# Kernel optimization log

Measured on AMD Instinct MI355X. Metric: run time of the kernel, lower is better.

The kernel has to match this reference:

```python
import jax, jax.numpy as jnp
import numpy as np
import math

DIM = 1024
N_HEADS = 16
HEAD_DIM = DIM // N_HEADS
MAX_LEN = 4096
THETA = 10000.0
LN_EPS = 1e-5


def _rope_tables(dim, max_len, theta=THETA):
    # matches precompute_rope: freqs over even indices, angles = outer(t, freqs)
    inv = 1.0 / theta ** (np.arange(0, dim, 2, dtype=np.float32) / dim)
    t = np.arange(max_len, dtype=np.float32)
    ang = np.outer(t, inv)  # [max_len, dim//2]
    return jnp.asarray(np.cos(ang)), jnp.asarray(np.sin(ang))


def setup_inputs() -> dict:
    key = jax.random.key(0)
    ks = jax.random.split(key, 5)
    B, T, D = 2, 2048, DIM
    s = 1.0 / math.sqrt(D)
    x = jax.random.normal(ks[0], (B, T, D), dtype=jnp.float32)
    wq = jax.random.normal(ks[1], (D, D), dtype=jnp.float32) * s
    wk = jax.random.normal(ks[2], (D, D), dtype=jnp.float32) * s
    wv = jax.random.normal(ks[3], (D, D), dtype=jnp.float32) * s
    wo = jax.random.normal(ks[4], (D, D), dtype=jnp.float32) * s
    ln_g = jnp.ones((D,), dtype=jnp.float32)
    ln_b = jnp.zeros((D,), dtype=jnp.float32)
    cos, sin = _rope_tables(HEAD_DIM, MAX_LEN)
    return {"x": x, "wq": wq, "wk": wk, "wv": wv, "wo": wo,
            "ln_g": ln_g, "ln_b": ln_b, "cos": cos, "sin": sin}


def _rotate(x, cos, sin):
    # x: [B, T, H, hd]; complex multiply on interleaved (even, odd) pairs
    B, T, H, hd = x.shape
    xr = x.reshape(B, T, H, hd // 2, 2)
    x0, x1 = xr[..., 0], xr[..., 1]
    c = cos[None, :T, None, :]
    s = sin[None, :T, None, :]
    o0 = x0 * c - x1 * s
    o1 = x0 * s + x1 * c
    return jnp.stack([o0, o1], axis=-1).reshape(B, T, H, hd)


def reference(x, wq, wk, wv, wo, ln_g, ln_b, cos, sin):
    B, T, D = x.shape
    H, hd = N_HEADS, HEAD_DIM
    # LayerNorm
    mu = jnp.mean(x, axis=-1, keepdims=True)
    var = jnp.var(x, axis=-1, keepdims=True)
    h = (x - mu) * jax.lax.rsqrt(var + LN_EPS) * ln_g + ln_b
    # QKV projections (torch Linear: h @ W.T)
    q = jnp.einsum('btd,ed->bte', h, wq).reshape(B, T, H, hd)
    k = jnp.einsum('btd,ed->bte', h, wk).reshape(B, T, H, hd)
    v = jnp.einsum('btd,ed->bte', h, wv).reshape(B, T, H, hd)
    q = _rotate(q, cos, sin)
    k = _rotate(k, cos, sin)
    # full (non-causal) attention, scores [B, H, T, T]
    scores = jnp.einsum('bqhd,bkhd->bhqk', q, k) / math.sqrt(hd)
    attn = jax.nn.softmax(scores, axis=-1)
    out = jnp.einsum('bhqk,bkhd->bqhd', attn, v).reshape(B, T, D)
    return jnp.einsum('btd,ed->bte', out, wo)
```

## Files before the change

kernel.cpp:

```cpp
#include <hip/hip_runtime.h>
#include <hip/hip_bf16.h>

typedef __attribute__((ext_vector_type(4))) float          fx4;
typedef __attribute__((ext_vector_type(8))) __bf16         bfx8;
typedef __attribute__((ext_vector_type(8))) unsigned short usx8;
typedef __attribute__((ext_vector_type(4))) unsigned short usx4;

#define TLEN 2048
#define ROWS 4096
#define D    1024

__device__ __forceinline__ float bf2f(unsigned short u) {
    union { unsigned int i; float f; } v; v.i = ((unsigned int)u) << 16; return v.f;
}
__device__ __forceinline__ unsigned short f2bf(float f) {
    union { float f; unsigned int i; } v; v.f = f;
    unsigned int r = v.i + 0x7fffu + ((v.i >> 16) & 1u);
    return (unsigned short)(r >> 16);
}
__device__ __forceinline__ unsigned int cvtpk_bf16(float lo, float hi) {
    unsigned int r;
    asm("v_cvt_pk_bf16_f32 %0, %1, %2" : "=v"(r) : "v"(lo), "v"(hi));
    return r;
}
__device__ __forceinline__ void gload_lds16(const unsigned short* g, unsigned short* l) {
    __builtin_amdgcn_global_load_lds((const __attribute__((address_space(1))) void*)g,
                                     (__attribute__((address_space(3))) void*)l, 16, 0, 0);
}

__device__ __forceinline__ usx4 cvt4(fx4 a) {
    usx4 o;
    #pragma unroll
    for (int j = 0; j < 4; j++) o[j] = f2bf(a[j]);
    return o;
}
__global__ __launch_bounds__(256) void prep_kernel(const float* __restrict__ x,
                                                   const float* __restrict__ g,
                                                   const float* __restrict__ bta,
                                                   const float* __restrict__ wq, const float* __restrict__ wk,
                                                   const float* __restrict__ wv, const float* __restrict__ wo,
                                                   unsigned short* __restrict__ hout,
                                                   unsigned short* __restrict__ wqkv,
                                                   unsigned short* __restrict__ wob,
                                                   float* __restrict__ ropeTab) {
    const int tid = threadIdx.x;
    if (blockIdx.x >= 5120) {
        const int idx = (blockIdx.x - 5120) * 256 + tid;
        const int pi_ = idx >> 11, t = idx & 2047;
        float inv = __builtin_amdgcn_exp2f(-0.415241011861f * (float)pi_);
        float ang = (float)t * inv;
        ropeTab[idx * 2]     = cosf(ang);
        ropeTab[idx * 2 + 1] = sinf(ang);
        return;
    }
    if (blockIdx.x >= 4096) {
        const int i = (blockIdx.x - 4096) * 256 + tid;
        ((usx4*)wqkv)[i]          = cvt4(((const fx4*)wq)[i]);
        ((usx4*)wqkv)[262144 + i] = cvt4(((const fx4*)wk)[i]);
        ((usx4*)wqkv)[524288 + i] = cvt4(((const fx4*)wv)[i]);
        ((usx4*)wob)[i]           = cvt4(((const fx4*)wo)[i]);
        return;
    }
    const int row = blockIdx.x;
    fx4 v = ((const fx4*)(x + (size_t)row * D))[tid];
    float s  = v[0] + v[1] + v[2] + v[3];
    float s2 = v[0]*v[0] + v[1]*v[1] + v[2]*v[2] + v[3]*v[3];
    #pragma unroll
    for (int mk = 32; mk >= 1; mk >>= 1) { s += __shfl_xor(s, mk); s2 += __shfl_xor(s2, mk); }
    __shared__ float red[8];
    const int wave = tid >> 6, lane = tid & 63;
    if (lane == 0) { red[wave] = s; red[4 + wave] = s2; }
    __syncthreads();
    s  = red[0] + red[1] + red[2] + red[3];
    s2 = red[4] + red[5] + red[6] + red[7];
    float mu   = s * (1.0f / D);
    float var  = s2 * (1.0f / D) - mu * mu;
    float rstd = rsqrtf(var + 1e-5f);
    fx4 gv = ((const fx4*)g)[tid];
    fx4 bv = ((const fx4*)bta)[tid];
    usx4 o;
    #pragma unroll
    for (int j = 0; j < 4; j++) o[j] = f2bf((v[j] - mu) * rstd * gv[j] + bv[j]);
    ((usx4*)hout)[(size_t)row * 256 + tid] = o;
}

__global__ __launch_bounds__(512) void qkvt_gemm(const unsigned short* __restrict__ hbuf,
                                                 const unsigned short* __restrict__ wqkv,
                                                 unsigned short* __restrict__ qkout,
                                                 unsigned short* __restrict__ vtout,
                                                 const float* __restrict__ ropeTab) {
    constexpr int K = 1024;
    __shared__ __align__(16) unsigned short As[2][256 * 64];
    __shared__ __align__(16) unsigned short Bs[2][256 * 64];
    const int tid = threadIdx.x, lane = tid & 63, wave = tid >> 6;
    const int fr = lane & 15, fq = lane >> 4;
    const int wr = wave >> 2, wc = wave & 3;

    const int id = (blockIdx.x & 7) * 24 + (blockIdx.x >> 3);
    const bool isqk = id < 128;
    int bm, bn;
    const unsigned short *Ab, *Bb;
    if (isqk) {
        bm = id & 15; bn = id >> 4;
        Ab = hbuf + (size_t)(bm * 256) * K;
        Bb = wqkv + (size_t)(bn * 256) * K;
    } else {
        int j = id - 128; bm = j & 3; bn = j >> 2;
        Ab = wqkv + (size_t)(2048 * 1024) + (size_t)(bm * 256) * K;
        Bb = hbuf + (size_t)(bn * 256) * K;
    }

    const int srow   = wave * 8 + (lane >> 3);
    const int sc_dst = (lane & 7) * 8;
    const int sc_src = ((lane & 7) ^ (lane >> 3)) * 8;

    #define STAGE_Q(BUF, KT)                                                          \
        {                                                                             \
            _Pragma("unroll")                                                         \
            for (int i = 0; i < 4; i++) {                                             \
                const int r = srow + 64 * i;                                          \
                gload_lds16(Ab + (size_t)r * K + (KT) + sc_src, &As[BUF][r * 64 + sc_dst]); \
                gload_lds16(Bb + (size_t)r * K + (KT) + sc_src, &Bs[BUF][r * 64 + sc_dst]); \
            }                                                                         \
        }

    fx4 acc[8][4];
    #pragma unroll
    for (int m = 0; m < 8; m++)
        #pragma unroll
        for (int n = 0; n < 4; n++) acc[m][n] = (fx4)0.0f;

    STAGE_Q(0, 0)

    #pragma unroll 2
    for (int kt = 0; kt < K; kt += 64) {
        const int b = (kt >> 6) & 1;
        __syncthreads();
        if (kt + 64 < K) STAGE_Q(b ^ 1, kt + 64)
        #pragma unroll
        for (int s = 0; s < 2; s++) {
            bfx8 aF[8], bF[4];
            #pragma unroll
            for (int m = 0; m < 8; m++)
                aF[m] = *(const bfx8*)&As[b][(wr * 128 + m * 16 + fr) * 64 + (((s * 4 + fq) ^ (fr & 7)) * 8)];
            #pragma unroll
            for (int n = 0; n < 4; n++)
                bF[n] = *(const bfx8*)&Bs[b][(wc * 64 + n * 16 + fr) * 64 + (((s * 4 + fq) ^ (fr & 7)) * 8)];
            #pragma unroll
            for (int m = 0; m < 8; m++)
                #pragma unroll
                for (int n = 0; n < 4; n++)
                    acc[m][n] = __builtin_amdgcn_mfma_f32_16x16x32_bf16(aF[m], bF[n], acc[m][n], 0, 0, 0);
        }
    }
    #undef STAGE_Q

    const int row0 = bm * 256 + wr * 128 + fq * 4;
    const int col0 = bn * 256 + wc * 64 + fr;
    if (isqk) {
        const float QS = 0.125f * 1.44269504088896f;
        const bool isq = bn < 4;
        const float sgn = (fr & 1) ? 1.0f : -1.0f;
        #pragma unroll
        for (int m = 0; m < 8; m++) {
            const int rbase = row0 + m * 16;
            const int tb = rbase & (TLEN - 1);
            #pragma unroll
            for (int n = 0; n < 4; n++) {
                const float* tp = ropeTab + ((((n * 8 + (fr >> 1)) << 11) | tb) << 1);
                fx4 csA = *(const fx4*)tp;
                fx4 csB = *(const fx4*)(tp + 4);
                #pragma unroll
                for (int j = 0; j < 4; j++) {
                    float c  = (j < 2) ? csA[2 * j]     : csB[2 * (j - 2)];
                    float s_ = (j < 2) ? csA[2 * j + 1] : csB[2 * (j - 2) + 1];
                    float self = acc[m][n][j];
                    float other = __shfl_xor(self, 1);
                    float o = self * c + other * (sgn * s_);
                    if (isq) o *= QS;
                    qkout[(size_t)(rbase + j) * 2048 + col0 + n * 16] = f2bf(o);
                }
            }
        }
    } else {
        const int bb = bn >> 3;
        #pragma unroll
        for (int m = 0; m < 8; m++)
            #pragma unroll
            for (int n = 0; n < 4; n++) {
                const int t = (col0 + n * 16) & (TLEN - 1);
                const int tp = (t & ~63) | ((n >> 1) * 32 + ((fr >> 2)) * 8 + ((n & 1)) * 4 + (fr & 3));
                #pragma unroll
                for (int j = 0; j < 4; j++) {
                    const int d = row0 + m * 16 + j;
                    vtout[(((size_t)(bb * 16 + (d >> 6)) * 64) + (d & 63)) * TLEN + tp] = f2bf(acc[m][n][j]);
                }
            }
    }
}

__global__ __launch_bounds__(256) void gemm_out64(const unsigned short* __restrict__ A,
                                                  const unsigned short* __restrict__ B,
                                                  float* __restrict__ C) {
    constexpr int K = 1024;
    __shared__ __align__(16) unsigned short As[128 * 64];
    __shared__ __align__(16) unsigned short Bs[64 * 64];
    const int tid = threadIdx.x, lane = tid & 63, wave = tid >> 6;
    const int fr = lane & 15, fq = lane >> 4;
    const int bm = blockIdx.x, bn = blockIdx.y;
    const int wr = wave >> 1, wc = wave & 1;

    const int srow   = wave * 8 + (lane >> 3);
    const int sc_dst = (lane & 7) * 8;
    const int sc_src = ((lane & 7) ^ (lane >> 3)) * 8;
    const unsigned short* Ab = A + (size_t)(bm * 128) * K;
    const unsigned short* Bb = B + (size_t)(bn * 64) * K;

    fx4 acc[4][2];
    #pragma unroll
    for (int m = 0; m < 4; m++)
        #pragma unroll
        for (int n = 0; n < 2; n++) acc[m][n] = (fx4)0.0f;

    for (int kt = 0; kt < K; kt += 64) {
        #pragma unroll
        for (int i = 0; i < 4; i++) {
            const int r = srow + 32 * i;
            gload_lds16(Ab + (size_t)r * K + kt + sc_src, &As[r * 64 + sc_dst]);
            if (i < 2)
                gload_lds16(Bb + (size_t)r * K + kt + sc_src, &Bs[r * 64 + sc_dst]);
        }
        __syncthreads();
        #pragma unroll
        for (int s = 0; s < 2; s++) {
            bfx8 aF[4], bF[2];
            #pragma unroll
            for (int m = 0; m < 4; m++)
                aF[m] = *(const bfx8*)&As[(wr * 64 + m * 16 + fr) * 64 + (((s * 4 + fq) ^ (fr & 7)) * 8)];
            #pragma unroll
            for (int n = 0; n < 2; n++)
                bF[n] = *(const bfx8*)&Bs[(wc * 32 + n * 16 + fr) * 64 + (((s * 4 + fq) ^ (fr & 7)) * 8)];
            #pragma unroll
            for (int m = 0; m < 4; m++)
                #pragma unroll
                for (int n = 0; n < 2; n++)
                    acc[m][n] = __builtin_amdgcn_mfma_f32_16x16x32_bf16(aF[m], bF[n], acc[m][n], 0, 0, 0);
        }
        __syncthreads();
    }

    const int row0 = bm * 128 + wr * 64 + fq * 4;
    const int col0 = bn * 64 + wc * 32 + fr;
    #pragma unroll
    for (int m = 0; m < 4; m++)
        #pragma unroll
        for (int n = 0; n < 2; n++)
            #pragma unroll
            for (int j = 0; j < 4; j++)
                C[(size_t)(row0 + m * 16 + j) * 1024 + col0 + n * 16] = acc[m][n][j];
}

__global__ __launch_bounds__(512) void attn_kernel(const unsigned short* __restrict__ qk,
                                                   const unsigned short* __restrict__ vt,
                                                   unsigned short* __restrict__ ao) {
    const int flat = blockIdx.x + (blockIdx.y << 3);
    const int sid  = (flat & 7) * 32 + (flat >> 3);
    const int qt = sid & 7, bh = sid >> 3;
    const int b = bh >> 4, hh = bh & 15;
    const int tid = threadIdx.x, lane = tid & 63, wave = tid >> 6;
    const int fr = lane & 15, fq = lane >> 4;

    __shared__ __align__(16) unsigned short sK[2][128 * 64];
    __shared__ __align__(16) unsigned short sVt[2][2 * 64 * 64];

    const size_t rs = 2048;
    const unsigned short* qb  = qk + (size_t)b * TLEN * rs + hh * 64;
    const unsigned short* kb  = qb + 1024;
    const unsigned short* vtb = vt + (size_t)bh * (64 * TLEN);

    bfx8 qF[2][2];
    #pragma unroll
    for (int g = 0; g < 2; g++) {
        int qrow = qt * 256 + wave * 32 + g * 16 + fr;
        const unsigned short* qp = qb + (size_t)qrow * rs + fq * 8;
        qF[g][0] = *(const bfx8*)qp;
        qF[g][1] = *(const bfx8*)(qp + 32);
    }
    union { unsigned short us[8]; bfx8 bf; } ones_u;
    #pragma unroll
    for (int i = 0; i < 8; i++) ones_u.us[i] = 0x3F80;

    const int srow = lane >> 3;
    const int scol = ((lane & 7) ^ srow) * 8;

    #define STAGE_ATTN(BUF, KT)                                                          \
        {                                                                                \
            _Pragma("unroll")                                                            \
            for (int i = 0; i < 2; i++) {                                                \
                const int rg = wave * 2 + i;                                             \
                gload_lds16(kb + (size_t)((KT) + rg * 8 + srow) * rs + scol,             \
                            &sK[BUF][rg * 512 + lane * 8]);                              \
                const int sub = rg >> 3, drow = (rg & 7) * 8 + srow;                     \
                gload_lds16(vtb + (size_t)drow * TLEN + (KT) + sub * 64 + scol,          \
                            &sVt[BUF][rg * 512 + lane * 8]);                             \
            }                                                                            \
        }

    STAGE_ATTN(0, 0)

    fx4 oacc[2][4];
    fx4 oextra[2] = {(fx4)0.0f, (fx4)0.0f};
    #pragma unroll
    for (int g = 0; g < 2; g++)
        #pragma unroll
        for (int db = 0; db < 4; db++) oacc[g][db] = (fx4)0.0f;

    #pragma unroll 2
    for (int t = 0; t < 16; ++t) {
        const int buf = t & 1;
        __syncthreads();

        if (t + 1 < 16) STAGE_ATTN(buf ^ 1, (t + 1) * 128)

        fx4 s0[8], s1[8];
        #pragma unroll
        for (int n = 0; n < 8; n++) { s0[n] = (fx4)0.0f; s1[n] = (fx4)0.0f; }
        __builtin_amdgcn_s_setprio(1);
        #pragma unroll
        for (int s = 0; s < 2; s++)
            #pragma unroll
            for (int n = 0; n < 8; n++) {
                bfx8 kF = *(const bfx8*)&sK[buf][(n * 16 + fr) * 64 + (((s * 4 + fq) ^ (fr & 7)) * 8)];
                s0[n] = __builtin_amdgcn_mfma_f32_16x16x32_bf16(kF, qF[0][s], s0[n], 0, 0, 0);
                s1[n] = __builtin_amdgcn_mfma_f32_16x16x32_bf16(kF, qF[1][s], s1[n], 0, 0, 0);
            }
        __builtin_amdgcn_s_setprio(0);

        unsigned int u0[8][2], u1[8][2];
        #pragma unroll
        for (int n = 0; n < 8; n++) {
            u0[n][0] = cvtpk_bf16(__builtin_amdgcn_exp2f(s0[n][0]), __builtin_amdgcn_exp2f(s0[n][1]));
            u0[n][1] = cvtpk_bf16(__builtin_amdgcn_exp2f(s0[n][2]), __builtin_amdgcn_exp2f(s0[n][3]));
        }

        __builtin_amdgcn_s_setprio(1);
        #pragma unroll
        for (int sp = 0; sp < 4; sp++) {
            union { unsigned int ui[4]; bfx8 bf; } cv;
            cv.ui[0] = u0[2 * sp][0];     cv.ui[1] = u0[2 * sp][1];
            cv.ui[2] = u0[2 * sp + 1][0]; cv.ui[3] = u0[2 * sp + 1][1];
            #pragma unroll
            for (int db = 0; db < 4; db++) {
                bfx8 vF = *(const bfx8*)&sVt[buf][(sp >> 1) * 4096 + (db * 16 + fr) * 64 +
                                                 ((((sp & 1) * 4 + fq) ^ (fr & 7)) * 8)];
                oacc[0][db] = __builtin_amdgcn_mfma_f32_16x16x32_bf16(vF, cv.bf, oacc[0][db], 0, 0, 0);
            }
            oextra[0] = __builtin_amdgcn_mfma_f32_16x16x32_bf16(ones_u.bf, cv.bf, oextra[0], 0, 0, 0);
        }
        __builtin_amdgcn_s_setprio(0);

        #pragma unroll
        for (int n = 0; n < 8; n++) {
            u1[n][0] = cvtpk_bf16(__builtin_amdgcn_exp2f(s1[n][0]), __builtin_amdgcn_exp2f(s1[n][1]));
            u1[n][1] = cvtpk_bf16(__builtin_amdgcn_exp2f(s1[n][2]), __builtin_amdgcn_exp2f(s1[n][3]));
        }

        __builtin_amdgcn_s_setprio(1);
        #pragma unroll
        for (int sp = 0; sp < 4; sp++) {
            union { unsigned int ui[4]; bfx8 bf; } cv;
            cv.ui[0] = u1[2 * sp][0];     cv.ui[1] = u1[2 * sp][1];
            cv.ui[2] = u1[2 * sp + 1][0]; cv.ui[3] = u1[2 * sp + 1][1];
            #pragma unroll
            for (int db = 0; db < 4; db++) {
                bfx8 vF = *(const bfx8*)&sVt[buf][(sp >> 1) * 4096 + (db * 16 + fr) * 64 +
                                                 ((((sp & 1) * 4 + fq) ^ (fr & 7)) * 8)];
                oacc[1][db] = __builtin_amdgcn_mfma_f32_16x16x32_bf16(vF, cv.bf, oacc[1][db], 0, 0, 0);
            }
            oextra[1] = __builtin_amdgcn_mfma_f32_16x16x32_bf16(ones_u.bf, cv.bf, oextra[1], 0, 0, 0);
        }
        __builtin_amdgcn_s_setprio(0);
    }
    #undef STAGE_ATTN

    #pragma unroll
    for (int g = 0; g < 2; g++) {
        float invl = 1.0f / oextra[g][0];
        const int qrow = qt * 256 + wave * 32 + g * 16 + fr;
        unsigned short* aop = ao + (size_t)(b * TLEN + qrow) * 1024 + hh * 64 + fq * 4;
        #pragma unroll
        for (int db = 0; db < 4; db++) {
            usx4 o4;
            #pragma unroll
            for (int j = 0; j < 4; j++) o4[j] = f2bf(oacc[g][db][j] * invl);
            *(usx4*)(aop + db * 16) = o4;
        }
    }
}

extern "C" void kernel_launch(void* const* d_in, const int* in_sizes, int n_in,
                              void* d_out, int out_size, void* d_ws, size_t ws_size,
                              hipStream_t stream) {
    const float* x    = (const float*)d_in[0];
    const float* wq   = (const float*)d_in[1];
    const float* wk   = (const float*)d_in[2];
    const float* wv   = (const float*)d_in[3];
    const float* wo   = (const float*)d_in[4];
    const float* lng  = (const float*)d_in[5];
    const float* lnb  = (const float*)d_in[6];

    char* ws = (char*)d_ws;
    unsigned short* wob  = (unsigned short*)(ws);
    unsigned short* wqkv = (unsigned short*)(ws + (2u  << 20));
    unsigned short* hbuf = (unsigned short*)(ws + (8u  << 20));
    unsigned short* qk   = (unsigned short*)(ws + (16u << 20));
    unsigned short* vtb  = (unsigned short*)(ws + (32u << 20));
    unsigned short* ao   = (unsigned short*)(ws + (8u  << 20));
    float* ropeTab = (float*)d_out;

    prep_kernel<<<5632, 256, 0, stream>>>(x, lng, lnb, wq, wk, wv, wo, hbuf, wqkv, wob, ropeTab);
    qkvt_gemm<<<192, 512, 0, stream>>>(hbuf, wqkv, qk, vtb, ropeTab);
    attn_kernel<<<dim3(8, 32), 512, 0, stream>>>(qk, vtb, ao);
    gemm_out64<<<dim3(32, 16), 256, 0, stream>>>(ao, wob, (float*)d_out);
}
```

Baseline: 107.4 us.

## Interleave QKV GEMM loads with four-phase MFMA compute and wave priority

Splits each K-tile of the QKV projection GEMM into four compute phases over 4x2 sub-blocks of the accumulator. The next tile's global-to-LDS loads are issued in four chunks between those phases, with explicit vmcnt waits and barriers replacing the single __syncthreads. s_setprio is raised around the MFMA bursts. The goal is to overlap memory issue with matrix work and smooth instruction scheduling. The cost is more barriers per tile and manual waitcnt logic that must stay correct.

```diff
diff --git a/kernel.cpp b/kernel.cpp
--- a/kernel.cpp
+++ b/kernel.cpp
@@ -114,14 +114,40 @@
     const int sc_dst = (lane & 7) * 8;
     const int sc_src = ((lane & 7) ^ (lane >> 3)) * 8;
 
-    #define STAGE_Q(BUF, KT)                                                          \
-        {                                                                             \
-            _Pragma("unroll")                                                         \
-            for (int i = 0; i < 4; i++) {                                             \
-                const int r = srow + 64 * i;                                          \
-                gload_lds16(Ab + (size_t)r * K + (KT) + sc_src, &As[BUF][r * 64 + sc_dst]); \
-                gload_lds16(Bb + (size_t)r * K + (KT) + sc_src, &Bs[BUF][r * 64 + sc_dst]); \
-            }                                                                         \
+    #define STAGE_UNIT(BUF, KT, U)                                                         \
+        {                                                                                  \
+            const unsigned short* _src = ((U) < 2) ? Ab : Bb;                              \
+            unsigned short* _dst = ((U) < 2) ? &As[BUF][0] : &Bs[BUF][0];                  \
+            const int _r0 = srow + (((U) & 1) ? 128 : 0);                                  \
+            gload_lds16(_src + (size_t)_r0 * K + (KT) + sc_src, _dst + _r0 * 64 + sc_dst); \
+            gload_lds16(_src + (size_t)(_r0 + 64) * K + (KT) + sc_src,                     \
+                        _dst + (_r0 + 64) * 64 + sc_dst);                                  \
+        }
+
+    #define PHASE_COMPUTE(B_, MH, NH)                                                      \
+        {                                                                                  \
+            bfx8 aF[2][4], bF[2][2];                                                       \
+            _Pragma("unroll")                                                              \
+            for (int s = 0; s < 2; s++) {                                                  \
+                _Pragma("unroll")                                                          \
+                for (int m = 0; m < 4; m++)                                                \
+                    aF[s][m] = *(const bfx8*)&As[B_][(wr * 128 + (MH) * 64 + m * 16 + fr) * 64 + \
+                                                    (((s * 4 + fq) ^ (fr & 7)) * 8)];      \
+                _Pragma("unroll")                                                          \
+                for (int n = 0; n < 2; n++)                                                \
+                    bF[s][n] = *(const bfx8*)&Bs[B_][(wc * 64 + (NH) * 32 + n * 16 + fr) * 64 + \
+                                                    (((s * 4 + fq) ^ (fr & 7)) * 8)];      \
+            }                                                                              \
+            __builtin_amdgcn_s_setprio(1);                                                 \
+            _Pragma("unroll")                                                              \
+            for (int s = 0; s < 2; s++)                                                    \
+                _Pragma("unroll")                                                          \
+                for (int m = 0; m < 4; m++)                                                \
+                    _Pragma("unroll")                                                      \
+                    for (int n = 0; n < 2; n++)                                            \
+                        acc[(MH) * 4 + m][(NH) * 2 + n] = __builtin_amdgcn_mfma_f32_16x16x32_bf16( \
+                            aF[s][m], bF[s][n], acc[(MH) * 4 + m][(NH) * 2 + n], 0, 0, 0); \
+            __builtin_amdgcn_s_setprio(0);                                                 \
         }
 
     fx4 acc[8][4];
@@ -130,30 +156,33 @@
         #pragma unroll
         for (int n = 0; n < 4; n++) acc[m][n] = (fx4)0.0f;
 
-    STAGE_Q(0, 0)
+    STAGE_UNIT(0, 0, 0) STAGE_UNIT(0, 0, 1) STAGE_UNIT(0, 0, 2) STAGE_UNIT(0, 0, 3)
 
     #pragma unroll 2
     for (int kt = 0; kt < K; kt += 64) {
         const int b = (kt >> 6) & 1;
-        __syncthreads();
-        if (kt + 64 < K) STAGE_Q(b ^ 1, kt + 64)
-        #pragma unroll
-        for (int s = 0; s < 2; s++) {
-            bfx8 aF[8], bF[4];
-            #pragma unroll
-            for (int m = 0; m < 8; m++)
-                aF[m] = *(const bfx8*)&As[b][(wr * 128 + m * 16 + fr) * 64 + (((s * 4 + fq) ^ (fr & 7)) * 8)];
-            #pragma unroll
-            for (int n = 0; n < 4; n++)
-                bF[n] = *(const bfx8*)&Bs[b][(wc * 64 + n * 16 + fr) * 64 + (((s * 4 + fq) ^ (fr & 7)) * 8)];
-            #pragma unroll
-            for (int m = 0; m < 8; m++)
-                #pragma unroll
-                for (int n = 0; n < 4; n++)
-                    acc[m][n] = __builtin_amdgcn_mfma_f32_16x16x32_bf16(aF[m], bF[n], acc[m][n], 0, 0, 0);
-        }
-    }
-    #undef STAGE_Q
+        const bool more = (kt + 64 < K);
+        if (more) {
+            STAGE_UNIT(b ^ 1, kt + 64, 0)
+            asm volatile("s_waitcnt vmcnt(2)" ::: "memory");
+        } else {
+            asm volatile("s_waitcnt vmcnt(0)" ::: "memory");
+        }
+        __builtin_amdgcn_s_barrier();
+        PHASE_COMPUTE(b, 0, 0)
+        if (more) STAGE_UNIT(b ^ 1, kt + 64, 1)
+        __builtin_amdgcn_s_barrier();
+        PHASE_COMPUTE(b, 0, 1)
+        if (more) STAGE_UNIT(b ^ 1, kt + 64, 2)
+        __builtin_amdgcn_s_barrier();
+        PHASE_COMPUTE(b, 1, 0)
+        if (more) STAGE_UNIT(b ^ 1, kt + 64, 3)
+        __builtin_amdgcn_s_barrier();
+        PHASE_COMPUTE(b, 1, 1)
+        __builtin_amdgcn_s_barrier();
+    }
+    #undef STAGE_UNIT
+    #undef PHASE_COMPUTE
 
     const int row0 = bm * 256 + wr * 128 + fq * 4;
     const int col0 = bn * 256 + wc * 64 + fr;
```

New measurement: 109.0 us. About the same (+1.4%).
